# Optimization experiments

Hardware: AMD Instinct MI355X
Metric: run time of the kernel (lower is better)

The kernel has to match this reference:

```python
import jax, jax.numpy as jnp
import numpy as np

B = 16384
IN = 128
H = 128
NC = 10
NATT = 3
EPS = 1e-5


def setup_inputs() -> dict:
    key = jax.random.key(0)
    ks = jax.random.split(key, 8)
    s_in = 1.0 / np.sqrt(IN)
    s_h = 1.0 / np.sqrt(H)
    return {
        "x": jax.random.normal(ks[0], (B, IN), dtype=jnp.float32),
        "W_in": jax.random.uniform(ks[1], (IN, H), jnp.float32, -s_in, s_in),
        "b_in": jax.random.uniform(ks[2], (H,), jnp.float32, -s_in, s_in),
        "W_att": jax.random.uniform(ks[3], (NATT, H, H), jnp.float32, -s_h, s_h),
        "b_att": jax.random.uniform(ks[4], (NATT, H), jnp.float32, -s_h, s_h),
        "gamma": jnp.ones((NATT, H), jnp.float32),
        "beta": jnp.zeros((NATT, H), jnp.float32),
        "W_c": jax.random.uniform(ks[5], (H, NC), jnp.float32, -s_h, s_h),
        "b_c": jax.random.uniform(ks[6], (NC,), jnp.float32, -s_h, s_h),
    }


def _layernorm(y, g, b):
    mu = jnp.mean(y, axis=-1, keepdims=True)
    var = jnp.mean((y - mu) ** 2, axis=-1, keepdims=True)
    return (y - mu) * jax.lax.rsqrt(var + EPS) * g + b


def reference(x, W_in, b_in, W_att, b_att, gamma, beta, W_c, b_c):
    # in_proj: [B, IN] -> [B, H]
    h = x @ W_in + b_in
    for i in range(NATT):
        u = jnp.tanh(h @ W_att[i] + b_att[i])            # [B, H]
        scores = u[:, :, None] * u[:, None, :]            # outer product [B, H, H]
        attn = jax.nn.softmax(scores, axis=-1)
        out = jnp.einsum("bij,bj->bi", attn, h)          # [B, H]
        h = _layernorm(h + out, gamma[i], beta[i])
    return h @ W_c + b_c                                  # [B, NC]
```

## Files before the change

### kernel.cpp

```cpp
#include <hip/hip_runtime.h>
#include <math.h>

#define B_TOT 16384
#define H     128
#define NC    10
#define NATT  3
#define TR    16
#define HBS   136
#define KT    5
#define EPS   1e-5f
#define EXM_CS 196
#define EXL_CS 34

typedef __attribute__((ext_vector_type(8))) short bf16x8;
typedef __attribute__((ext_vector_type(4))) float f32x4;

__device__ __forceinline__ ushort f2bf(float f) {
    union { float f; unsigned u; } v; v.f = f;
    unsigned r = v.u + 0x7fffu + ((v.u >> 16) & 1u);
    return (ushort)(r >> 16);
}

__device__ __forceinline__ float fast_tanh(float a) {
    float t = __expf(2.f * a);
    return 1.f - 2.f * __builtin_amdgcn_rcpf(t + 1.f);
}

template<int CTRL>
__device__ __forceinline__ float dpp_add(float v) {
    int x = __float_as_int(v);
    int y = __builtin_amdgcn_update_dpp(0, x, CTRL, 0xf, 0xf, false);
    return v + __int_as_float(y);
}
__device__ __forceinline__ float red16(float v) {
    v = dpp_add<0x121>(v);
    v = dpp_add<0x122>(v);
    v = dpp_add<0x124>(v);
    v = dpp_add<0x128>(v);
    return v;
}
__device__ __forceinline__ float red8ror(float v) {
    v = dpp_add<0x121>(v);
    v = dpp_add<0x122>(v);
    v = dpp_add<0x124>(v);
    return v;
}

extern "C" __global__ __launch_bounds__(256)
void prep_weights(const float* __restrict__ W_in,
                  const float* __restrict__ W_att,
                  const float* __restrict__ W_c,
                  ushort* __restrict__ wt)
{
    int i = blockIdx.x * 256 + threadIdx.x;
    if (i < 65536) {
        int mat = i >> 14, idx = i & 16383;
        int k = idx >> 7, n = idx & 127;
        float v = (mat == 0) ? W_in[idx] : W_att[(mat - 1) * 16384 + idx];
        wt[mat * 16384 + n * H + k] = f2bf(v);
    } else if (i < 65536 + 2048) {
        int idx = i - 65536;
        int n = idx >> 7, k = idx & 127;
        float v = (n < NC) ? W_c[k * NC + n] : 0.f;
        wt[65536 + n * H + k] = f2bf(v);
    }
}

extern "C" __global__ __launch_bounds__(512, 6)
void simple_attention_kernel(const float* __restrict__ x,
                             const float* __restrict__ b_in,
                             const float* __restrict__ b_att,
                             const float* __restrict__ gamma,
                             const float* __restrict__ beta,
                             const float* __restrict__ b_c,
                             const ushort* __restrict__ wt,
                             float* __restrict__ out)
{
    __shared__ __align__(16) ushort ab[TR * HBS];
    __shared__ __align__(16) float  exm[8 * EXM_CS];
    __shared__ __align__(16) float  exl[8 * EXL_CS];

    const int tid  = threadIdx.x;
    const int wv   = tid >> 6;
    const int lane = tid & 63;
    const int s    = lane & 15;
    const int q    = lane >> 4;
    const size_t rowBase = (size_t)blockIdx.x * TR;
    const int colN = 16 * wv + s;

    float h[4];
    f32x4 acc;

    if (wv < 4) {
        const float* xp = x + (rowBase + s) * H + 32 * wv + q * 8;
        float4 v0 = *(const float4*)xp;
        float4 v1 = *(const float4*)(xp + 4);
        bf16x8 a;
        a[0] = f2bf(v0.x); a[1] = f2bf(v0.y); a[2] = f2bf(v0.z); a[3] = f2bf(v0.w);
        a[4] = f2bf(v1.x); a[5] = f2bf(v1.y); a[6] = f2bf(v1.z); a[7] = f2bf(v1.w);
        *(bf16x8*)&ab[s * HBS + 32 * wv + q * 8] = a;
    }
    __syncthreads();

    {
        bf16x8 af[4];
        #pragma unroll
        for (int ks = 0; ks < 4; ++ks)
            af[ks] = *(const bf16x8*)&ab[s * HBS + ks * 32 + q * 8];
        acc = (f32x4){0.f, 0.f, 0.f, 0.f};
        #pragma unroll
        for (int ks = 0; ks < 4; ++ks) {
            bf16x8 b = *(const bf16x8*)&wt[colN * H + ks * 32 + q * 8];
            acc = __builtin_amdgcn_mfma_f32_16x16x32_bf16(af[ks], b, acc, 0, 0, 0);
        }
        __syncthreads();
        float bi = b_in[colN];
        #pragma unroll
        for (int r = 0; r < 4; ++r) {
            h[r] = acc[r] + bi;
            ab[(4 * q + r) * HBS + colN] = f2bf(h[r]);
        }
        __syncthreads();
    }

    const float cm[KT] = {1.00004478f, 0.99730768f, 0.49919676f, 0.17734736f, 0.04379392f};

    #pragma unroll 1
    for (int layer = 0; layer < NATT; ++layer) {
        const ushort* WT = wt + (size_t)(1 + layer) * 16384;

        bf16x8 af[4];
        #pragma unroll
        for (int ks = 0; ks < 4; ++ks)
            af[ks] = *(const bf16x8*)&ab[s * HBS + ks * 32 + q * 8];
        acc = (f32x4){0.f, 0.f, 0.f, 0.f};
        #pragma unroll
        for (int ks = 0; ks < 4; ++ks) {
            bf16x8 b = *(const bf16x8*)&WT[colN * H + ks * 32 + q * 8];
            acc = __builtin_amdgcn_mfma_f32_16x16x32_bf16(af[ks], b, acc, 0, 0, 0);
        }
        float ba = b_att[layer * H + colN];
        float u[4];
        #pragma unroll
        for (int r = 0; r < 4; ++r) u[r] = fast_tanh(acc[r] + ba);

        #pragma unroll
        for (int r = 0; r < 4; ++r) {
            float uu = u[r], hh = h[r];
            float m0 = hh;
            float p  = uu;
            float m1 = p * hh, t0 = p;
            p *= uu; float m2 = p * hh, t1 = p;
            p *= uu; float m3 = p * hh, t2 = p;
            p *= uu; float m4 = p * hh, t3 = p;
            m0 = red16(m0); m1 = red16(m1); m2 = red16(m2);
            m3 = red16(m3); m4 = red16(m4);
            t0 = red16(t0); t1 = red16(t1); t2 = red16(t2); t3 = red16(t3);
            if (s == 0) {
                float* dst = &exm[wv * EXM_CS + (4 * q + r) * 12];
                *(f32x4*)&dst[0] = (f32x4){m0, m1, m2, m3};
                *(f32x4*)&dst[4] = (f32x4){m4, t0, t1, t2};
                dst[8] = t3;
            }
        }
        __syncthreads();

        #pragma unroll
        for (int r = 0; r < 4; ++r) {
            const float* src = &exm[(s & 7) * EXM_CS + (4 * q + r) * 12];
            f32x4 c0 = *(const f32x4*)&src[0];
            f32x4 c1 = *(const f32x4*)&src[4];
            float c2 = src[8];
            float S0 = red8ror(c0.x) * cm[0];
            float S1 = red8ror(c0.y) * cm[1];
            float S2 = red8ror(c0.z) * cm[2];
            float S3 = red8ror(c0.w) * cm[3];
            float S4 = red8ror(c1.x) * cm[4];
            float T0 = red8ror(c1.y) * cm[1];
            float T1 = red8ror(c1.z) * cm[2];
            float T2 = red8ror(c1.w) * cm[3];
            float T3 = red8ror(c2)   * cm[4];
            float uu = u[r];
            float num = fmaf(fmaf(fmaf(fmaf(S4, uu, S3), uu, S2), uu, S1), uu, S0);
            float den = fmaf(fmaf(fmaf(fmaf(T3, uu, T2), uu, T1), uu, T0), uu,
                             128.f * 1.00004478f);
            float yy = h[r] + num * __builtin_amdgcn_rcpf(den);
            h[r] = yy;
            float lsv = red16(yy);
            float lqv = red16(yy * yy);
            if (s == 0)
                *(float2*)&exl[wv * EXL_CS + (4 * q + r) * 2] = make_float2(lsv, lqv);
        }
        __syncthreads();

        float g  = gamma[layer * H + colN];
        float be = beta [layer * H + colN];
        #pragma unroll
        for (int r = 0; r < 4; ++r) {
            float2 o = *(const float2*)&exl[(s & 7) * EXL_CS + (4 * q + r) * 2];
            float sm = red8ror(o.x), sq = red8ror(o.y);
            float mu = sm * (1.f / H);
            float var = sq * (1.f / H) - mu * mu;
            float inv = rsqrtf(var + EPS);
            float hn = (h[r] - mu) * inv * g + be;
            h[r] = hn;
            ab[(4 * q + r) * HBS + colN] = f2bf(hn);
        }
        __syncthreads();
    }

    if (wv == 0) {
        const ushort* WC = wt + 4 * 16384;
        f32x4 facc = (f32x4){0.f, 0.f, 0.f, 0.f};
        #pragma unroll
        for (int ks = 0; ks < 4; ++ks) {
            bf16x8 a = *(const bf16x8*)&ab[s * HBS + ks * 32 + q * 8];
            bf16x8 b = *(const bf16x8*)&WC[s * H + ks * 32 + q * 8];
            facc = __builtin_amdgcn_mfma_f32_16x16x32_bf16(a, b, facc, 0, 0, 0);
        }
        if (s < NC) {
            float bc = b_c[s];
            #pragma unroll
            for (int r = 0; r < 4; ++r)
                out[(rowBase + 4 * q + r) * NC + s] = facc[r] + bc;
        }
    }
}

extern "C" void kernel_launch(void* const* d_in, const int* in_sizes, int n_in,
                              void* d_out, int out_size, void* d_ws, size_t ws_size,
                              hipStream_t stream) {
    const float* x     = (const float*)d_in[0];
    const float* W_in  = (const float*)d_in[1];
    const float* b_in  = (const float*)d_in[2];
    const float* W_att = (const float*)d_in[3];
    const float* b_att = (const float*)d_in[4];
    const float* gamma = (const float*)d_in[5];
    const float* beta  = (const float*)d_in[6];
    const float* W_c   = (const float*)d_in[7];
    const float* b_c   = (const float*)d_in[8];
    float* out  = (float*)d_out;
    ushort* wt  = (ushort*)d_ws;

    hipLaunchKernelGGL(prep_weights, dim3(264), dim3(256), 0, stream,
                       W_in, W_att, W_c, wt);
    hipLaunchKernelGGL(simple_attention_kernel, dim3(B_TOT / TR), dim3(512), 0, stream,
                       x, b_in, b_att, gamma, beta, b_c, wt, out);
}
```

Before: 114.1 us.

## Transpose MFMA operands so each lane owns one row's four features

```diff
diff --git a/kernel.cpp b/kernel.cpp
--- a/kernel.cpp
+++ b/kernel.cpp
@@ -9,8 +9,8 @@
 #define HBS   136
 #define KT    5
 #define EPS   1e-5f
-#define EXM_CS 196
-#define EXL_CS 34
+#define EXM_S 100
+#define EXL_S 20
 
 typedef __attribute__((ext_vector_type(8))) short bf16x8;
 typedef __attribute__((ext_vector_type(4))) float f32x4;
@@ -26,23 +26,9 @@
     return 1.f - 2.f * __builtin_amdgcn_rcpf(t + 1.f);
 }
 
-template<int CTRL>
-__device__ __forceinline__ float dpp_add(float v) {
-    int x = __float_as_int(v);
-    int y = __builtin_amdgcn_update_dpp(0, x, CTRL, 0xf, 0xf, false);
-    return v + __int_as_float(y);
-}
-__device__ __forceinline__ float red16(float v) {
-    v = dpp_add<0x121>(v);
-    v = dpp_add<0x122>(v);
-    v = dpp_add<0x124>(v);
-    v = dpp_add<0x128>(v);
-    return v;
-}
-__device__ __forceinline__ float red8ror(float v) {
-    v = dpp_add<0x121>(v);
-    v = dpp_add<0x122>(v);
-    v = dpp_add<0x124>(v);
+__device__ __forceinline__ float redq(float v) {
+    v += __shfl_xor(v, 16);
+    v += __shfl_xor(v, 32);
     return v;
 }
 
@@ -77,16 +63,16 @@
                              float* __restrict__ out)
 {
     __shared__ __align__(16) ushort ab[TR * HBS];
-    __shared__ __align__(16) float  exm[8 * EXM_CS];
-    __shared__ __align__(16) float  exl[8 * EXL_CS];
+    __shared__ __align__(16) float  exm[16 * EXM_S];
+    __shared__ __align__(16) float  exl[16 * EXL_S];
 
     const int tid  = threadIdx.x;
     const int wv   = tid >> 6;
     const int lane = tid & 63;
     const int s    = lane & 15;
     const int q    = lane >> 4;
+    const int nq   = 16 * wv + 4 * q;
     const size_t rowBase = (size_t)blockIdx.x * TR;
-    const int colN = 16 * wv + s;
 
     float h[4];
     f32x4 acc;
@@ -103,23 +89,27 @@
     __syncthreads();
 
     {
-        bf16x8 af[4];
+        bf16x8 bfr[4];
         #pragma unroll
         for (int ks = 0; ks < 4; ++ks)
-            af[ks] = *(const bf16x8*)&ab[s * HBS + ks * 32 + q * 8];
+            bfr[ks] = *(const bf16x8*)&ab[s * HBS + ks * 32 + q * 8];
         acc = (f32x4){0.f, 0.f, 0.f, 0.f};
         #pragma unroll
         for (int ks = 0; ks < 4; ++ks) {
-            bf16x8 b = *(const bf16x8*)&wt[colN * H + ks * 32 + q * 8];
-            acc = __builtin_amdgcn_mfma_f32_16x16x32_bf16(af[ks], b, acc, 0, 0, 0);
-        }
-        __syncthreads();
-        float bi = b_in[colN];
-        #pragma unroll
-        for (int r = 0; r < 4; ++r) {
-            h[r] = acc[r] + bi;
-            ab[(4 * q + r) * HBS + colN] = f2bf(h[r]);
-        }
+            bf16x8 a = *(const bf16x8*)&wt[(16 * wv + s) * H + ks * 32 + q * 8];
+            acc = __builtin_amdgcn_mfma_f32_16x16x32_bf16(a, bfr[ks], acc, 0, 0, 0);
+        }
+        __syncthreads();
+        float4 bi4 = *(const float4*)&b_in[nq];
+        uint lo, hi;
+        {
+            float h0 = acc[0] + bi4.x, h1 = acc[1] + bi4.y;
+            float h2 = acc[2] + bi4.z, h3 = acc[3] + bi4.w;
+            h[0] = h0; h[1] = h1; h[2] = h2; h[3] = h3;
+            lo = (uint)f2bf(h0) | ((uint)f2bf(h1) << 16);
+            hi = (uint)f2bf(h2) | ((uint)f2bf(h3) << 16);
+        }
+        *(uint2*)&ab[s * HBS + nq] = make_uint2(lo, hi);
         __syncthreads();
     }
 
@@ -129,82 +119,100 @@
     for (int layer = 0; layer < NATT; ++layer) {
         const ushort* WT = wt + (size_t)(1 + layer) * 16384;
 
-        bf16x8 af[4];
+        bf16x8 bfr[4];
         #pragma unroll
         for (int ks = 0; ks < 4; ++ks)
-            af[ks] = *(const bf16x8*)&ab[s * HBS + ks * 32 + q * 8];
+            bfr[ks] = *(const bf16x8*)&ab[s * HBS + ks * 32 + q * 8];
         acc = (f32x4){0.f, 0.f, 0.f, 0.f};
         #pragma unroll
         for (int ks = 0; ks < 4; ++ks) {
-            bf16x8 b = *(const bf16x8*)&WT[colN * H + ks * 32 + q * 8];
-            acc = __builtin_amdgcn_mfma_f32_16x16x32_bf16(af[ks], b, acc, 0, 0, 0);
-        }
-        float ba = b_att[layer * H + colN];
+            bf16x8 a = *(const bf16x8*)&WT[(16 * wv + s) * H + ks * 32 + q * 8];
+            acc = __builtin_amdgcn_mfma_f32_16x16x32_bf16(a, bfr[ks], acc, 0, 0, 0);
+        }
+        float4 ba4 = *(const float4*)&b_att[layer * H + nq];
         float u[4];
-        #pragma unroll
-        for (int r = 0; r < 4; ++r) u[r] = fast_tanh(acc[r] + ba);
-
+        u[0] = fast_tanh(acc[0] + ba4.x);
+        u[1] = fast_tanh(acc[1] + ba4.y);
+        u[2] = fast_tanh(acc[2] + ba4.z);
+        u[3] = fast_tanh(acc[3] + ba4.w);
+
+        float m0 = 0, m1 = 0, m2 = 0, m3 = 0, m4 = 0;
+        float t1 = 0, t2 = 0, t3 = 0, t4 = 0;
         #pragma unroll
         for (int r = 0; r < 4; ++r) {
             float uu = u[r], hh = h[r];
-            float m0 = hh;
-            float p  = uu;
-            float m1 = p * hh, t0 = p;
-            p *= uu; float m2 = p * hh, t1 = p;
-            p *= uu; float m3 = p * hh, t2 = p;
-            p *= uu; float m4 = p * hh, t3 = p;
-            m0 = red16(m0); m1 = red16(m1); m2 = red16(m2);
-            m3 = red16(m3); m4 = red16(m4);
-            t0 = red16(t0); t1 = red16(t1); t2 = red16(t2); t3 = red16(t3);
-            if (s == 0) {
-                float* dst = &exm[wv * EXM_CS + (4 * q + r) * 12];
-                *(f32x4*)&dst[0] = (f32x4){m0, m1, m2, m3};
-                *(f32x4*)&dst[4] = (f32x4){m4, t0, t1, t2};
-                dst[8] = t3;
-            }
-        }
-        __syncthreads();
-
+            m0 += hh;
+            float p = uu;
+            m1 += p * hh; t1 += p;
+            p *= uu; m2 += p * hh; t2 += p;
+            p *= uu; m3 += p * hh; t3 += p;
+            p *= uu; m4 += p * hh; t4 += p;
+        }
+        m0 = redq(m0); m1 = redq(m1); m2 = redq(m2); m3 = redq(m3); m4 = redq(m4);
+        t1 = redq(t1); t2 = redq(t2); t3 = redq(t3); t4 = redq(t4);
+        {
+            float* dst = &exm[s * EXM_S + wv * 12];
+            if (q == 0)      *(f32x4*)&dst[0] = (f32x4){m0, m1, m2, m3};
+            else if (q == 1) *(f32x4*)&dst[4] = (f32x4){m4, t1, t2, t3};
+            else if (q == 2) *(f32x4*)&dst[8] = (f32x4){t4, 0.f, 0.f, 0.f};
+        }
+        __syncthreads();
+
+        float S0, S1, S2, S3, S4, T1c, T2c, T3c, T4c;
+        {
+            const float* src = &exm[s * EXM_S + 24 * q];
+            f32x4 a0 = *(const f32x4*)&src[0];
+            f32x4 a1 = *(const f32x4*)&src[4];
+            f32x4 a2 = *(const f32x4*)&src[8];
+            f32x4 b0 = *(const f32x4*)&src[12];
+            f32x4 b1 = *(const f32x4*)&src[16];
+            f32x4 b2 = *(const f32x4*)&src[20];
+            a0 += b0; a1 += b1; a2 += b2;
+            S0  = redq(a0.x) * cm[0];
+            S1  = redq(a0.y) * cm[1];
+            S2  = redq(a0.z) * cm[2];
+            S3  = redq(a0.w) * cm[3];
+            S4  = redq(a1.x) * cm[4];
+            T1c = redq(a1.y) * cm[1];
+            T2c = redq(a1.z) * cm[2];
+            T3c = redq(a1.w) * cm[3];
+            T4c = redq(a2.x) * cm[4];
+        }
+
+        float ls = 0.f, lq2 = 0.f;
         #pragma unroll
         for (int r = 0; r < 4; ++r) {
-            const float* src = &exm[(s & 7) * EXM_CS + (4 * q + r) * 12];
-            f32x4 c0 = *(const f32x4*)&src[0];
-            f32x4 c1 = *(const f32x4*)&src[4];
-            float c2 = src[8];
-            float S0 = red8ror(c0.x) * cm[0];
-            float S1 = red8ror(c0.y) * cm[1];
-            float S2 = red8ror(c0.z) * cm[2];
-            float S3 = red8ror(c0.w) * cm[3];
-            float S4 = red8ror(c1.x) * cm[4];
-            float T0 = red8ror(c1.y) * cm[1];
-            float T1 = red8ror(c1.z) * cm[2];
-            float T2 = red8ror(c1.w) * cm[3];
-            float T3 = red8ror(c2)   * cm[4];
             float uu = u[r];
             float num = fmaf(fmaf(fmaf(fmaf(S4, uu, S3), uu, S2), uu, S1), uu, S0);
-            float den = fmaf(fmaf(fmaf(fmaf(T3, uu, T2), uu, T1), uu, T0), uu,
+            float den = fmaf(fmaf(fmaf(fmaf(T4c, uu, T3c), uu, T2c), uu, T1c), uu,
                              128.f * 1.00004478f);
             float yy = h[r] + num * __builtin_amdgcn_rcpf(den);
             h[r] = yy;
-            float lsv = red16(yy);
-            float lqv = red16(yy * yy);
-            if (s == 0)
-                *(float2*)&exl[wv * EXL_CS + (4 * q + r) * 2] = make_float2(lsv, lqv);
-        }
-        __syncthreads();
-
-        float g  = gamma[layer * H + colN];
-        float be = beta [layer * H + colN];
-        #pragma unroll
-        for (int r = 0; r < 4; ++r) {
-            float2 o = *(const float2*)&exl[(s & 7) * EXL_CS + (4 * q + r) * 2];
-            float sm = red8ror(o.x), sq = red8ror(o.y);
-            float mu = sm * (1.f / H);
-            float var = sq * (1.f / H) - mu * mu;
+            ls += yy; lq2 += yy * yy;
+        }
+        ls  = redq(ls);
+        lq2 = redq(lq2);
+        if (q == 0)
+            *(float2*)&exl[s * EXL_S + wv * 2] = make_float2(ls, lq2);
+        __syncthreads();
+
+        {
+            f32x4 rd = *(const f32x4*)&exl[s * EXL_S + 4 * q];
+            float sm  = redq(rd.x + rd.z);
+            float sq2 = redq(rd.y + rd.w);
+            float mu  = sm * (1.f / H);
+            float var = sq2 * (1.f / H) - mu * mu;
             float inv = rsqrtf(var + EPS);
-            float hn = (h[r] - mu) * inv * g + be;
-            h[r] = hn;
-            ab[(4 * q + r) * HBS + colN] = f2bf(hn);
+            float4 g4  = *(const float4*)&gamma[layer * H + nq];
+            float4 be4 = *(const float4*)&beta [layer * H + nq];
+            float h0 = (h[0] - mu) * inv * g4.x + be4.x;
+            float h1 = (h[1] - mu) * inv * g4.y + be4.y;
+            float h2 = (h[2] - mu) * inv * g4.z + be4.z;
+            float h3 = (h[3] - mu) * inv * g4.w + be4.w;
+            h[0] = h0; h[1] = h1; h[2] = h2; h[3] = h3;
+            uint lo = (uint)f2bf(h0) | ((uint)f2bf(h1) << 16);
+            uint hi = (uint)f2bf(h2) | ((uint)f2bf(h3) << 16);
+            *(uint2*)&ab[s * HBS + nq] = make_uint2(lo, hi);
         }
         __syncthreads();
     }
```

After: 100.6 us. -11.8%, faster.
